# Kernel tuning notes

Hardware: AMD Instinct MI355X
Metric: run time of the kernel (lower is better)

## Reference

```python
import jax, jax.numpy as jnp
import numpy as np

NUM_HEADS = 8
N_WIN = 8
TOPK = 4
DIM = 256


def setup_inputs() -> dict:
    key = jax.random.key(0)
    ks = jax.random.split(key, 5)
    B, T, H, W = 16, 16, 16, 16
    N = T * H * W
    x = jax.random.normal(ks[0], (B, N, DIM), dtype=jnp.float32)
    w_qkv = jax.random.normal(ks[1], (DIM, 3 * DIM), dtype=jnp.float32) * (DIM ** -0.5)
    b_qkv = jnp.zeros((3 * DIM,), dtype=jnp.float32)
    w_proj = jax.random.normal(ks[2], (DIM, DIM), dtype=jnp.float32) * (DIM ** -0.5)
    b_proj = jnp.zeros((DIM,), dtype=jnp.float32)
    return {"x": x, "w_qkv": w_qkv, "b_qkv": b_qkv, "w_proj": w_proj,
            "b_proj": b_proj, "T": T, "H": H, "W": W}


def reference(x, w_qkv, b_qkv, w_proj, b_proj, T, H, W):
    B, N, C = x.shape
    h = NUM_HEADS
    d = C // h
    scale = d ** -0.5
    S = H * W

    # qkv projection -> [3, B, T, h, S, d]
    qkv = (x.reshape(B, T, S, C) @ w_qkv + b_qkv).reshape(B, T, S, 3, h, d)
    qkv = jnp.transpose(qkv, (3, 0, 1, 4, 2, 5))
    q, k, v = qkv[0], qkv[1], qkv[2]

    n_win = N_WIN if S % N_WIN == 0 else S
    win = S // n_win
    qr = q.reshape(B, T, h, n_win, win, d)
    kr = k.reshape(B, T, h, n_win, win, d)
    vr = v.reshape(B, T, h, n_win, win, d)

    # spike-driven region features: sum over window tokens
    q_reg = qr.sum(axis=4)  # [B,T,h,n_win,d]
    k_reg = kr.sum(axis=4)
    sim = jnp.einsum('bthnd,bthmd->bthnm', q_reg, k_reg) * scale

    # mask out dead (non-firing) key regions
    activity = jnp.abs(kr).sum(axis=(4, 5))  # [B,T,h,n_win]
    act_mask = (activity > 1e-5).astype(sim.dtype)
    sim = sim + (1.0 - act_mask)[:, :, :, None, :] * -1e9

    tk = min(TOPK, n_win)
    _, idx = jax.lax.top_k(sim, tk)  # [B,T,h,n_win,tk]

    gidx = (idx[..., None] * win + jnp.arange(win)).reshape(B, T, h, n_win, tk * win)

    k_flat = kr.reshape(B, T, h, S, d)
    v_flat = vr.reshape(B, T, h, S, d)
    kg = jnp.take_along_axis(k_flat[:, :, :, None], gidx[..., None], axis=4)
    vg = jnp.take_along_axis(v_flat[:, :, :, None], gidx[..., None], axis=4)

    attn = jnp.einsum('bthnwd,bthngd->bthnwg', qr, kg) * scale
    attn = jax.nn.softmax(attn, axis=-1)
    out = jnp.einsum('bthnwg,bthngd->bthnwd', attn, vg)

    out = out.reshape(B, T, h, S, d).transpose(0, 1, 3, 2, 4).reshape(B, N, C)
    return out @ w_proj + b_proj
```

## Files before the change

kernel.cpp:

```cpp
#include <hip/hip_runtime.h>
#include <math.h>

constexpr int Bn   = 16;
constexpr int Tn   = 16;
constexpr int Sn   = 256;
constexpr int Cn   = 256;
constexpr int NH   = 8;
constexpr int HD   = 32;
constexpr int NW   = 8;
constexpr int WINW = 32;
constexpr float SCALE = 0.17677669529663687f;
constexpr float CEXP  = 0.2550756272475434f;

typedef __attribute__((ext_vector_type(8))) short bf16x8;
typedef __attribute__((ext_vector_type(4))) float f32x4;

__device__ inline float bf2f(unsigned short u) {
  return __uint_as_float(((unsigned int)u) << 16);
}
__device__ inline unsigned short f2bf(float f) {
  unsigned int u = __float_as_uint(f);
  u += 0x7FFFu + ((u >> 16) & 1u);
  return (unsigned short)(u >> 16);
}
__device__ inline unsigned int cvtpk_bf16(float lo, float hi) {
  unsigned int r;
  asm("v_cvt_pk_bf16_f32 %0, %1, %2" : "=v"(r) : "v"(lo), "v"(hi));
  return r;
}
__device__ inline float fast_exp2(float x) {
  float r;
  asm("v_exp_f32 %0, %1" : "=v"(r) : "v"(x));
  return r;
}
__device__ inline void gload16(const void* g, const void* l) {
  __builtin_amdgcn_global_load_lds(
      (const __attribute__((address_space(1))) void*)g,
      (__attribute__((address_space(3))) void*)l, 16, 0, 0);
}

__global__ __launch_bounds__(256) void k_prep(const float* __restrict__ x,
                                              const float* __restrict__ w_qkv,
                                              const float* __restrict__ w_proj,
                                              float* __restrict__ xs,
                                              unsigned short* __restrict__ xb,
                                              unsigned short* __restrict__ wtb,
                                              float* __restrict__ wtf,
                                              unsigned short* __restrict__ wpt) {
  __shared__ __align__(16) float psum[4][256];
  const int blk = blockIdx.x;
  const int tid = threadIdx.x;
  if (blk < 2048) {
    const size_t row0 = (size_t)blk * 32;
    const int rg = tid >> 6, cg = tid & 63;
    float4 s4 = {0.f, 0.f, 0.f, 0.f};
#pragma unroll
    for (int r = 0; r < 8; ++r) {
      const size_t row = row0 + rg * 8 + r;
      const float4 v = *(const float4*)(x + row * 256 + cg * 4);
      s4.x += v.x; s4.y += v.y; s4.z += v.z; s4.w += v.w;
      ushort4 u;
      u.x = f2bf(v.x); u.y = f2bf(v.y); u.z = f2bf(v.z); u.w = f2bf(v.w);
      *(ushort4*)(xb + row * 256 + cg * 4) = u;
    }
    *(float4*)&psum[rg][cg * 4] = s4;
    __syncthreads();
    const int c = tid;
    xs[(size_t)blk * 256 + c] =
        (psum[0][c] + psum[1][c]) + (psum[2][c] + psum[3][c]);
  } else if (blk < 2816) {
    const int co = blk - 2048;
    const float val = w_qkv[(size_t)tid * 768 + co];
    wtf[(size_t)co * 256 + tid] = val;
    wtb[(size_t)co * 256 + tid] = f2bf(val);
  } else {
    const int co = blk - 2816;
    wpt[(size_t)co * 256 + tid] = f2bf(w_proj[(size_t)tid * 256 + co]);
  }
}

__global__ __launch_bounds__(256) void k_regtopk(const float* __restrict__ xs,
                                                 const float* __restrict__ wtf,
                                                 const float* __restrict__ bias,
                                                 int* __restrict__ idxout) {
  __shared__ __align__(16) float xl[8][256];
  __shared__ __align__(16) float ql[8][256];
  __shared__ __align__(16) float kl[8][256];
  __shared__ float sim[8][8][8];
  const int bt = blockIdx.x;
  const int tid = threadIdx.x;
  {
    const float4* src = (const float4*)(xs + (size_t)bt * 2048);
    float4* dst = (float4*)&xl[0][0];
    dst[tid] = src[tid];
    dst[tid + 256] = src[tid + 256];
  }
  __syncthreads();
  {
    float accq[8] = {}, acck[8] = {};
    const float4* wq = (const float4*)(wtf + (size_t)tid * 256);
    const float4* wk = (const float4*)(wtf + (size_t)(256 + tid) * 256);
#pragma unroll 4
    for (int i = 0; i < 64; ++i) {
      const float4 a = wq[i];
      const float4 b = wk[i];
#pragma unroll
      for (int n = 0; n < 8; ++n) {
        const float4 xv = *(const float4*)&xl[n][i * 4];
        accq[n] = fmaf(xv.x, a.x,
                  fmaf(xv.y, a.y, fmaf(xv.z, a.z, fmaf(xv.w, a.w, accq[n]))));
        acck[n] = fmaf(xv.x, b.x,
                  fmaf(xv.y, b.y, fmaf(xv.z, b.z, fmaf(xv.w, b.w, acck[n]))));
      }
    }
    const float bq = 32.f * bias[tid];
    const float bk = 32.f * bias[256 + tid];
#pragma unroll
    for (int n = 0; n < 8; ++n) {
      ql[n][tid] = accq[n] + bq;
      kl[n][tid] = acck[n] + bk;
    }
  }
  __syncthreads();
  {
    const int h = tid >> 5, n = (tid >> 2) & 7, m0 = (tid & 3) * 2;
#pragma unroll
    for (int mm = 0; mm < 2; ++mm) {
      const int m = m0 + mm;
      float s = 0.f;
#pragma unroll
      for (int d = 0; d < 32; ++d)
        s = fmaf(ql[n][h * 32 + d], kl[m][h * 32 + d], s);
      sim[h][n][m] = s;
    }
  }
  __syncthreads();
  if (tid < 64) {
    const int h = tid >> 3, n = tid & 7;
    float vals[8];
#pragma unroll
    for (int m = 0; m < 8; ++m) vals[m] = sim[h][n][m];
#pragma unroll
    for (int j = 0; j < 4; ++j) {
      float best = -3.402823466e38f;
      int bi = 0;
#pragma unroll
      for (int m = 0; m < 8; ++m)
        if (vals[m] > best) { best = vals[m]; bi = m; }
      vals[bi] = -3.402823466e38f;
      idxout[(((size_t)bt * 8 + h) * 8 + n) * 4 + j] = bi;
    }
  }
}

__global__ __launch_bounds__(256) void k_qkv_mfma(
    const unsigned short* __restrict__ Xb,
    const unsigned short* __restrict__ Wt,
    const float* __restrict__ bias,
    unsigned short* __restrict__ q,
    unsigned short* __restrict__ k,
    unsigned short* __restrict__ v) {
  __shared__ short As[128 * 64];
  __shared__ short Bs[128 * 64];
  const int tid = threadIdx.x;
  const int wid = tid >> 6, lane = tid & 63;
  const int p = blockIdx.x;
  const int bidx = (p & 7) * 384 + (p >> 3);
  const int mt = bidx / 6, nt = bidx - mt * 6;
  const int row0 = mt * 128, col0 = nt * 128;
  const int wm = (wid >> 1) * 64, wn = (wid & 1) * 64;

  f32x4 acc[4][4] = {};

  const int lr = lane >> 3, lc = lane & 7;

  for (int kk0 = 0; kk0 < 256; kk0 += 64) {
#pragma unroll
    for (int j = 0; j < 4; ++j) {
      const int r = wid * 32 + j * 8 + lr;
      const int gsw = (lc ^ (r & 7)) * 8;
      gload16(Xb + (size_t)(row0 + r) * 256 + kk0 + gsw,
              (const char*)As + (wid * 32 + j * 8) * 128);
      gload16(Wt + (size_t)(col0 + r) * 256 + kk0 + gsw,
              (const char*)Bs + (wid * 32 + j * 8) * 128);
    }
    __syncthreads();

#pragma unroll
    for (int ks = 0; ks < 2; ++ks) {
      const int g = ks * 4 + (lane >> 4);
      bf16x8 af[4], bfr[4];
#pragma unroll
      for (int i = 0; i < 4; ++i) {
        const int rm = wm + i * 16 + (lane & 15);
        af[i] = *(const bf16x8*)((const char*)As + rm * 128 + 16 * (g ^ (rm & 7)));
        const int rn = wn + i * 16 + (lane & 15);
        bfr[i] = *(const bf16x8*)((const char*)Bs + rn * 128 + 16 * (g ^ (rn & 7)));
      }
#pragma unroll
      for (int i = 0; i < 4; ++i)
#pragma unroll
        for (int j = 0; j < 4; ++j)
          acc[i][j] = __builtin_amdgcn_mfma_f32_16x16x32_bf16(
              af[i], bfr[j], acc[i][j], 0, 0, 0);
    }
    __syncthreads();
  }

  const int cl = lane & 15, rg = lane >> 4;
#pragma unroll
  for (int j = 0; j < 4; ++j) {
    const int n = col0 + wn + j * 16 + cl;
    const float bia = bias[n];
    const int pp = n >> 8, hh = (n >> 5) & 7, dd = n & 31;
    unsigned short* dst = (pp == 0) ? q : (pp == 1) ? k : v;
#pragma unroll
    for (int i = 0; i < 4; ++i) {
      const int mbase = row0 + wm + i * 16 + rg * 4;
#pragma unroll
      for (int r = 0; r < 4; ++r) {
        const int m = mbase + r;
        const int bt = m >> 8, s = m & 255;
        dst[((size_t)(bt * NH + hh) * Sn + s) * HD + dd] = f2bf(acc[i][j][r] + bia);
      }
    }
  }
}

__global__ __launch_bounds__(256) void k_attn_mfma(
    const unsigned short* __restrict__ qb,
    const unsigned short* __restrict__ kb,
    const unsigned short* __restrict__ vb,
    const int* __restrict__ idx,
    unsigned short* __restrict__ ao) {
  __shared__ __align__(16) short kx[256 * 32];
  __shared__ __align__(16) short vt[32 * 264];
  __shared__ __align__(16) unsigned int pl[4][32 * 35];
  __shared__ float sbuf[4][32];
  const int bth = blockIdx.x;
  const int bt = bth >> 3, h = bth & 7;
  const int tid = threadIdx.x;
  const int wid = tid >> 6, l = tid & 63;
  const int g = l >> 4, q15 = l & 15;
  const unsigned short* kg = kb + (size_t)bth * 8192;
  const unsigned short* vg = vb + (size_t)bth * 8192;
  const unsigned short* qg = qb + (size_t)bth * 8192;

  {
    const int tloc = tid >> 2, cst = tid & 3;
#pragma unroll
    for (int it = 0; it < 4; ++it) {
      const int t = it * 64 + tloc;
      const int csrc = cst ^ ((t >> 1) & 3);
      gload16((const char*)kg + t * 64 + csrc * 16,
              (const char*)kx + it * 4096 + wid * 1024);
    }
  }
  {
    const int t = tid;
    unsigned short us[32];
#pragma unroll
    for (int i = 0; i < 4; ++i)
      *(int4*)(us + 8 * i) = ((const int4*)(vg + (size_t)t * 32))[i];
#pragma unroll
    for (int d = 0; d < 32; ++d) vt[d * 264 + t] = us[d];
  }
  __syncthreads();

#pragma unroll
  for (int ww = 0; ww < 2; ++ww) {
    const int wi = wid + ww * 4;
    const bf16x8 qf0 = *(const bf16x8*)(qg + (wi * 32 + q15) * 32 + g * 8);
    const bf16x8 qf1 = *(const bf16x8*)(qg + (wi * 32 + 16 + q15) * 32 + g * 8);
    const int4 s4 = *(const int4*)(idx + ((size_t)bth * 8 + wi) * 4);
    const int sel[4] = {s4.x, s4.y, s4.z, s4.w};

    f32x4 st[8][2] = {};
    __builtin_amdgcn_s_setprio(1);
#pragma unroll
    for (int mt = 0; mt < 8; ++mt) {
      const int t = sel[mt >> 1] * 32 + (mt & 1) * 16 + q15;
      const bf16x8 kf =
          *(const bf16x8*)((const char*)kx + t * 64 + (g ^ ((t >> 1) & 3)) * 16);
      st[mt][0] = __builtin_amdgcn_mfma_f32_16x16x32_bf16(kf, qf0, st[mt][0], 0, 0, 0);
      st[mt][1] = __builtin_amdgcn_mfma_f32_16x16x32_bf16(kf, qf1, st[mt][1], 0, 0, 0);
    }
    __builtin_amdgcn_s_setprio(0);

    float sm0 = 0.f, sm1 = 0.f;
#pragma unroll
    for (int mt = 0; mt < 8; ++mt)
#pragma unroll
      for (int r = 0; r < 4; ++r) {
        const float e0 = fast_exp2(st[mt][0][r] * CEXP);
        const float e1 = fast_exp2(st[mt][1][r] * CEXP);
        st[mt][0][r] = e0; sm0 += e0;
        st[mt][1][r] = e1; sm1 += e1;
      }
    sm0 += __shfl_xor(sm0, 16); sm0 += __shfl_xor(sm0, 32);
    sm1 += __shfl_xor(sm1, 16); sm1 += __shfl_xor(sm1, 32);
    sbuf[wid][q15] = sm0;
    sbuf[wid][16 + q15] = sm1;

    f32x4 oa[2][2] = {};
#pragma unroll
    for (int c = 0; c < 2; ++c) {
#pragma unroll
      for (int m3 = 0; m3 < 4; ++m3) {
        const int mt = c * 4 + m3;
        const int tl2 = m3 * 8 + 2 * g;
#pragma unroll
        for (int nt = 0; nt < 2; ++nt) {
          const int row = nt * 16 + q15;
          pl[wid][row * 35 + tl2]     = cvtpk_bf16(st[mt][nt][0], st[mt][nt][1]);
          pl[wid][row * 35 + tl2 + 1] = cvtpk_bf16(st[mt][nt][2], st[mt][nt][3]);
        }
      }
      __builtin_amdgcn_s_setprio(1);
#pragma unroll
      for (int a = 0; a < 2; ++a) {
        const bf16x8 pa0 = *(const bf16x8*)((const char*)&pl[wid][0] +
                                            q15 * 140 + (a * 32 + g * 8) * 2);
        const bf16x8 pa1 = *(const bf16x8*)((const char*)&pl[wid][0] +
                                            (16 + q15) * 140 + (a * 32 + g * 8) * 2);
        const int tv = sel[c * 2 + a] * 32 + g * 8;
#pragma unroll
        for (int nt = 0; nt < 2; ++nt) {
          const bf16x8 vf =
              *(const bf16x8*)((const char*)vt + (nt * 16 + q15) * 528 + tv * 2);
          oa[0][nt] = __builtin_amdgcn_mfma_f32_16x16x32_bf16(pa0, vf, oa[0][nt], 0, 0, 0);
          oa[1][nt] = __builtin_amdgcn_mfma_f32_16x16x32_bf16(pa1, vf, oa[1][nt], 0, 0, 0);
        }
      }
      __builtin_amdgcn_s_setprio(0);
    }

    const size_t rowbase = (size_t)bt * 256 + wi * 32;
#pragma unroll
    for (int mtO = 0; mtO < 2; ++mtO) {
      float inv[4];
#pragma unroll
      for (int r = 0; r < 4; ++r)
        inv[r] = __builtin_amdgcn_rcpf(sbuf[wid][mtO * 16 + g * 4 + r]);
#pragma unroll
      for (int nt = 0; nt < 2; ++nt)
#pragma unroll
        for (int r = 0; r < 4; ++r) {
          const size_t tok = rowbase + mtO * 16 + g * 4 + r;
          ao[tok * 256 + h * 32 + nt * 16 + q15] = f2bf(oa[mtO][nt][r] * inv[r]);
        }
    }
  }
}

__global__ __launch_bounds__(256) void k_proj_mfma(
    const unsigned short* __restrict__ AO,
    const unsigned short* __restrict__ Wp,
    const float* __restrict__ bias,
    float* __restrict__ out) {
  __shared__ short As[128 * 64];
  __shared__ short Bs[128 * 64];
  const int tid = threadIdx.x;
  const int wid = tid >> 6, lane = tid & 63;
  const int p = blockIdx.x;
  const int bidx = (p & 7) * 128 + (p >> 3);
  const int mt = bidx >> 1, nt = bidx & 1;
  const int row0 = mt * 128, col0 = nt * 128;
  const int wm = (wid >> 1) * 64, wn = (wid & 1) * 64;

  f32x4 acc[4][4] = {};
  const int lr = lane >> 3, lc = lane & 7;

  for (int kk0 = 0; kk0 < 256; kk0 += 64) {
#pragma unroll
    for (int j = 0; j < 4; ++j) {
      const int r = wid * 32 + j * 8 + lr;
      const int gsw = (lc ^ (r & 7)) * 8;
      gload16(AO + (size_t)(row0 + r) * 256 + kk0 + gsw,
              (const char*)As + (wid * 32 + j * 8) * 128);
      gload16(Wp + (size_t)(col0 + r) * 256 + kk0 + gsw,
              (const char*)Bs + (wid * 32 + j * 8) * 128);
    }
    __syncthreads();

#pragma unroll
    for (int ks = 0; ks < 2; ++ks) {
      const int g = ks * 4 + (lane >> 4);
      bf16x8 af[4], bfr[4];
#pragma unroll
      for (int i = 0; i < 4; ++i) {
        const int rm = wm + i * 16 + (lane & 15);
        af[i] = *(const bf16x8*)((const char*)As + rm * 128 + 16 * (g ^ (rm & 7)));
        const int rn = wn + i * 16 + (lane & 15);
        bfr[i] = *(const bf16x8*)((const char*)Bs + rn * 128 + 16 * (g ^ (rn & 7)));
      }
#pragma unroll
      for (int i = 0; i < 4; ++i)
#pragma unroll
        for (int j = 0; j < 4; ++j)
          acc[i][j] = __builtin_amdgcn_mfma_f32_16x16x32_bf16(
              af[i], bfr[j], acc[i][j], 0, 0, 0);
    }
    __syncthreads();
  }

  const int cl = lane & 15, rg = lane >> 4;
#pragma unroll
  for (int j = 0; j < 4; ++j) {
    const int n = col0 + wn + j * 16 + cl;
    const float bia = bias[n];
#pragma unroll
    for (int i = 0; i < 4; ++i) {
      const int mbase = row0 + wm + i * 16 + rg * 4;
#pragma unroll
      for (int r = 0; r < 4; ++r)
        out[(size_t)(mbase + r) * 256 + n] = acc[i][j][r] + bia;
    }
  }
}

extern "C" void kernel_launch(void* const* d_in, const int* in_sizes, int n_in,
                              void* d_out, int out_size, void* d_ws,
                              size_t ws_size, hipStream_t stream) {
  const float* x      = (const float*)d_in[0];
  const float* w_qkv  = (const float*)d_in[1];
  const float* b_qkv  = (const float*)d_in[2];
  const float* w_proj = (const float*)d_in[3];
  const float* b_proj = (const float*)d_in[4];
  float* out = (float*)d_out;

  char* ws = (char*)d_ws;
  unsigned short* xb  = (unsigned short*)(ws);
  unsigned short* ao  = (unsigned short*)(ws);
  unsigned short* q   = (unsigned short*)(ws + ((size_t)32 << 20));
  unsigned short* k   = (unsigned short*)(ws + ((size_t)64 << 20));
  unsigned short* v   = (unsigned short*)(ws + ((size_t)96 << 20));
  float*          xs  = (float*)(ws + ((size_t)128 << 20));
  unsigned short* wtb = (unsigned short*)(ws + ((size_t)131 << 20));
  unsigned short* wpt = (unsigned short*)(ws + ((size_t)131 << 20) + (512 << 10));
  float*          wtf = (float*)(ws + ((size_t)132 << 20));
  int*            idx = (int*)(ws + ((size_t)133 << 20));

  k_prep<<<3072, 256, 0, stream>>>(x, w_qkv, w_proj, xs, xb, wtb, wtf, wpt);
  k_regtopk<<<256, 256, 0, stream>>>(xs, wtf, b_qkv, idx);
  k_qkv_mfma<<<3072, 256, 0, stream>>>(xb, wtb, b_qkv, q, k, v);
  k_attn_mfma<<<2048, 256, 0, stream>>>(q, k, v, idx, ao);
  k_proj_mfma<<<1024, 256, 0, stream>>>(ao, wpt, b_proj, out);
}
```

Measured before the change: 139.3 us.

## Widen QKV GEMM tile to 128x256 and vectorize MFMA epilogue stores

The QKV GEMM tile grows from 128x128 to 128x256, so each wave computes a 64x128 sub-tile and the grid is halved. This raises reuse of the activation tile and cuts redundant A loads. The MFMA operands are swapped in the QKV, attention PV and projection kernels so each lane holds four consecutive output columns, which lets the epilogues use packed 8-byte bf16 or 16-byte float stores instead of scalar stores. The prep kernel is also simplified to per-thread column sums without shared memory, but its loads become scalar 4-byte accesses. The larger tile raises register and LDS use and may lower occupancy.

```diff
diff --git a/kernel.cpp b/kernel.cpp
--- a/kernel.cpp
+++ b/kernel.cpp
@@ -47,27 +47,18 @@
                                               unsigned short* __restrict__ wtb,
                                               float* __restrict__ wtf,
                                               unsigned short* __restrict__ wpt) {
-  __shared__ __align__(16) float psum[4][256];
   const int blk = blockIdx.x;
   const int tid = threadIdx.x;
   if (blk < 2048) {
     const size_t row0 = (size_t)blk * 32;
-    const int rg = tid >> 6, cg = tid & 63;
-    float4 s4 = {0.f, 0.f, 0.f, 0.f};
-#pragma unroll
-    for (int r = 0; r < 8; ++r) {
-      const size_t row = row0 + rg * 8 + r;
-      const float4 v = *(const float4*)(x + row * 256 + cg * 4);
-      s4.x += v.x; s4.y += v.y; s4.z += v.z; s4.w += v.w;
-      ushort4 u;
-      u.x = f2bf(v.x); u.y = f2bf(v.y); u.z = f2bf(v.z); u.w = f2bf(v.w);
-      *(ushort4*)(xb + row * 256 + cg * 4) = u;
-    }
-    *(float4*)&psum[rg][cg * 4] = s4;
-    __syncthreads();
-    const int c = tid;
-    xs[(size_t)blk * 256 + c] =
-        (psum[0][c] + psum[1][c]) + (psum[2][c] + psum[3][c]);
+    float acc = 0.f;
+#pragma unroll
+    for (int r = 0; r < 32; ++r) {
+      const float val = x[(row0 + r) * Cn + tid];
+      acc += val;
+      xb[(row0 + r) * Cn + tid] = f2bf(val);
+    }
+    xs[(size_t)blk * Cn + tid] = acc;
   } else if (blk < 2816) {
     const int co = blk - 2048;
     const float val = w_qkv[(size_t)tid * 768 + co];
@@ -161,16 +152,16 @@
     unsigned short* __restrict__ k,
     unsigned short* __restrict__ v) {
   __shared__ short As[128 * 64];
-  __shared__ short Bs[128 * 64];
+  __shared__ short Bs[256 * 64];
   const int tid = threadIdx.x;
   const int wid = tid >> 6, lane = tid & 63;
   const int p = blockIdx.x;
-  const int bidx = (p & 7) * 384 + (p >> 3);
-  const int mt = bidx / 6, nt = bidx - mt * 6;
-  const int row0 = mt * 128, col0 = nt * 128;
-  const int wm = (wid >> 1) * 64, wn = (wid & 1) * 64;
-
-  f32x4 acc[4][4] = {};
+  const int bidx = (p & 7) * 192 + (p >> 3);
+  const int mt = bidx / 3, nt = bidx - mt * 3;
+  const int row0 = mt * 128, col0 = nt * 256;
+  const int wm = (wid >> 1) * 64, wn = (wid & 1) * 128;
+
+  f32x4 acc[4][8] = {};
 
   const int lr = lane >> 3, lc = lane & 7;
 
@@ -181,48 +172,56 @@
       const int gsw = (lc ^ (r & 7)) * 8;
       gload16(Xb + (size_t)(row0 + r) * 256 + kk0 + gsw,
               (const char*)As + (wid * 32 + j * 8) * 128);
+    }
+#pragma unroll
+    for (int j = 0; j < 8; ++j) {
+      const int r = wid * 64 + j * 8 + lr;
+      const int gsw = (lc ^ (r & 7)) * 8;
       gload16(Wt + (size_t)(col0 + r) * 256 + kk0 + gsw,
-              (const char*)Bs + (wid * 32 + j * 8) * 128);
+              (const char*)Bs + (wid * 64 + j * 8) * 128);
     }
     __syncthreads();
 
 #pragma unroll
     for (int ks = 0; ks < 2; ++ks) {
       const int g = ks * 4 + (lane >> 4);
-      bf16x8 af[4], bfr[4];
+      bf16x8 af[4], bfr[8];
 #pragma unroll
       for (int i = 0; i < 4; ++i) {
         const int rm = wm + i * 16 + (lane & 15);
         af[i] = *(const bf16x8*)((const char*)As + rm * 128 + 16 * (g ^ (rm & 7)));
-        const int rn = wn + i * 16 + (lane & 15);
-        bfr[i] = *(const bf16x8*)((const char*)Bs + rn * 128 + 16 * (g ^ (rn & 7)));
+      }
+#pragma unroll
+      for (int j = 0; j < 8; ++j) {
+        const int rn = wn + j * 16 + (lane & 15);
+        bfr[j] = *(const bf16x8*)((const char*)Bs + rn * 128 + 16 * (g ^ (rn & 7)));
       }
 #pragma unroll
       for (int i = 0; i < 4; ++i)
 #pragma unroll
-        for (int j = 0; j < 4; ++j)
+        for (int j = 0; j < 8; ++j)
           acc[i][j] = __builtin_amdgcn_mfma_f32_16x16x32_bf16(
-              af[i], bfr[j], acc[i][j], 0, 0, 0);
+              bfr[j], af[i], acc[i][j], 0, 0, 0);
     }
     __syncthreads();
   }
 
-  const int cl = lane & 15, rg = lane >> 4;
-#pragma unroll
-  for (int j = 0; j < 4; ++j) {
-    const int n = col0 + wn + j * 16 + cl;
-    const float bia = bias[n];
-    const int pp = n >> 8, hh = (n >> 5) & 7, dd = n & 31;
+  const int tkl = lane & 15, rg = lane >> 4;
+#pragma unroll
+  for (int j = 0; j < 8; ++j) {
+    const int n0 = col0 + wn + j * 16 + rg * 4;
+    const float4 bia = *reinterpret_cast<const float4*>(bias + n0);
+    const int pp = n0 >> 8, hh = (n0 >> 5) & 7, dd = n0 & 31;
     unsigned short* dst = (pp == 0) ? q : (pp == 1) ? k : v;
 #pragma unroll
     for (int i = 0; i < 4; ++i) {
-      const int mbase = row0 + wm + i * 16 + rg * 4;
-#pragma unroll
-      for (int r = 0; r < 4; ++r) {
-        const int m = mbase + r;
-        const int bt = m >> 8, s = m & 255;
-        dst[((size_t)(bt * NH + hh) * Sn + s) * HD + dd] = f2bf(acc[i][j][r] + bia);
-      }
+      const int m = row0 + wm + i * 16 + tkl;
+      const int bt = m >> 8, s = m & 255;
+      uint2 o;
+      o.x = cvtpk_bf16(acc[i][j][0] + bia.x, acc[i][j][1] + bia.y);
+      o.y = cvtpk_bf16(acc[i][j][2] + bia.z, acc[i][j][3] + bia.w);
+      *reinterpret_cast<uint2*>(
+          dst + ((size_t)(bt * NH + hh) * Sn + s) * HD + dd) = o;
     }
   }
 }
@@ -328,27 +327,27 @@
         for (int nt = 0; nt < 2; ++nt) {
           const bf16x8 vf =
               *(const bf16x8*)((const char*)vt + (nt * 16 + q15) * 528 + tv * 2);
-          oa[0][nt] = __builtin_amdgcn_mfma_f32_16x16x32_bf16(pa0, vf, oa[0][nt], 0, 0, 0);
-          oa[1][nt] = __builtin_amdgcn_mfma_f32_16x16x32_bf16(pa1, vf, oa[1][nt], 0, 0, 0);
+          oa[0][nt] = __builtin_amdgcn_mfma_f32_16x16x32_bf16(vf, pa0, oa[0][nt], 0, 0, 0);
+          oa[1][nt] = __builtin_amdgcn_mfma_f32_16x16x32_bf16(vf, pa1, oa[1][nt], 0, 0, 0);
         }
       }
       __builtin_amdgcn_s_setprio(0);
     }
 
     const size_t rowbase = (size_t)bt * 256 + wi * 32;
+    const int rg = g;
 #pragma unroll
     for (int mtO = 0; mtO < 2; ++mtO) {
-      float inv[4];
-#pragma unroll
-      for (int r = 0; r < 4; ++r)
-        inv[r] = __builtin_amdgcn_rcpf(sbuf[wid][mtO * 16 + g * 4 + r]);
-#pragma unroll
-      for (int nt = 0; nt < 2; ++nt)
-#pragma unroll
-        for (int r = 0; r < 4; ++r) {
-          const size_t tok = rowbase + mtO * 16 + g * 4 + r;
-          ao[tok * 256 + h * 32 + nt * 16 + q15] = f2bf(oa[mtO][nt][r] * inv[r]);
-        }
+      const float inv = __builtin_amdgcn_rcpf(sbuf[wid][mtO * 16 + q15]);
+      const size_t tok = rowbase + mtO * 16 + q15;
+#pragma unroll
+      for (int nt = 0; nt < 2; ++nt) {
+        uint2 o;
+        o.x = cvtpk_bf16(oa[mtO][nt][0] * inv, oa[mtO][nt][1] * inv);
+        o.y = cvtpk_bf16(oa[mtO][nt][2] * inv, oa[mtO][nt][3] * inv);
+        *reinterpret_cast<uint2*>(
+            ao + tok * 256 + h * 32 + nt * 16 + rg * 4) = o;
+      }
     }
   }
 }
@@ -399,22 +398,23 @@
 #pragma unroll
         for (int j = 0; j < 4; ++j)
           acc[i][j] = __builtin_amdgcn_mfma_f32_16x16x32_bf16(
-              af[i], bfr[j], acc[i][j], 0, 0, 0);
+              bfr[j], af[i], acc[i][j], 0, 0, 0);
     }
     __syncthreads();
   }
 
-  const int cl = lane & 15, rg = lane >> 4;
+  const int tkl = lane & 15, rg = lane >> 4;
 #pragma unroll
   for (int j = 0; j < 4; ++j) {
-    const int n = col0 + wn + j * 16 + cl;
-    const float bia = bias[n];
+    const int n0 = col0 + wn + j * 16 + rg * 4;
+    const float4 bia = *reinterpret_cast<const float4*>(bias + n0);
 #pragma unroll
     for (int i = 0; i < 4; ++i) {
-      const int mbase = row0 + wm + i * 16 + rg * 4;
-#pragma unroll
-      for (int r = 0; r < 4; ++r)
-        out[(size_t)(mbase + r) * 256 + n] = acc[i][j][r] + bia;
+      const int m = row0 + wm + i * 16 + tkl;
+      float4 o;
+      o.x = acc[i][j][0] + bia.x; o.y = acc[i][j][1] + bia.y;
+      o.z = acc[i][j][2] + bia.z; o.w = acc[i][j][3] + bia.w;
+      *reinterpret_cast<float4*>(out + (size_t)m * 256 + n0) = o;
     }
   }
 }
@@ -443,7 +443,7 @@
 
   k_prep<<<3072, 256, 0, stream>>>(x, w_qkv, w_proj, xs, xb, wtb, wtf, wpt);
   k_regtopk<<<256, 256, 0, stream>>>(xs, wtf, b_qkv, idx);
-  k_qkv_mfma<<<3072, 256, 0, stream>>>(xb, wtb, b_qkv, q, k, v);
+  k_qkv_mfma<<<1536, 256, 0, stream>>>(xb, wtb, b_qkv, q, k, v);
   k_attn_mfma<<<2048, 256, 0, stream>>>(q, k, v, idx, ao);
   k_proj_mfma<<<1024, 256, 0, stream>>>(ao, wpt, b_proj, out);
 }
```

New measurement: 163.0 us. 1.17x slower.
